# Performance work log

Hardware: AMD Instinct MI355X
Metric: run time of the kernel (lower is better)

## Reference

```python
import jax, jax.numpy as jnp
import numpy as np

H = 256; S = 64; AN = 16; D = 8; HH = 8; WW = 8; T = 32; N = 64; NV = 32
HG = 2 + 3 * H  # GRU hidden = sum(parser_sections) = 1 + 1 + 3*H


def _gru(x, w_ih, w_hh, b_ih, b_hh):
    """torch-style GRU over leading axis; x: [L, N, Hin] -> [L, N, HG]."""
    def step(h, xt):
        gi = xt @ w_ih.T + b_ih
        gh = h @ w_hh.T + b_hh
        ir, iz, inn = jnp.split(gi, 3, axis=-1)
        hr, hz, hn = jnp.split(gh, 3, axis=-1)
        r = jax.nn.sigmoid(ir + hr)
        z = jax.nn.sigmoid(iz + hz)
        n = jnp.tanh(inn + r * hn)
        h2 = (1 - z) * n + z * h
        return h2, h2
    h0 = jnp.zeros((x.shape[1], w_hh.shape[1]), x.dtype)
    _, ys = jax.lax.scan(step, h0, x)
    return ys


def _cos(e, m):  # e [N,H], m [N,S,H] -> [N,S]; matches F.cosine_similarity eps=1e-8
    num = jnp.einsum('nh,nsh->ns', e, m)
    den = jnp.linalg.norm(e, axis=-1)[:, None] * jnp.linalg.norm(m, axis=-1)
    return num / jnp.maximum(den, 1e-8)


def _l1norm(x):  # F.normalize(x, p=1, dim=-1)
    return x / jnp.maximum(jnp.abs(x).sum(-1, keepdims=True), 1e-12)


def setup_inputs():
    key = jax.random.key(0)
    ks = jax.random.split(key, 16)
    sc = lambda k, shape, fan: jax.random.normal(k, shape, jnp.float32) / np.float32(np.sqrt(fan))
    return dict(
        base=jax.random.normal(ks[0], (T, N, D, HH, WW), jnp.float32),
        interactable=(jax.random.uniform(ks[1], (T, N, AN - 5)) < 0.5).astype(jnp.float32),
        rnn_hxs=jnp.zeros((1, N, 1 + AN + 1 + H + S), jnp.float32),
        emb=sc(ks[2], (NV, H), 1.0),
        gru_w_ih=sc(ks[3], (3 * HG, H), H),
        gru_w_hh=sc(ks[4], (3 * HG, HG), HG),
        gru_b_ih=jnp.zeros((3 * HG,), jnp.float32),
        gru_b_hh=jnp.zeros((3 * HG,), jnp.float32),
        conv0_w=sc(ks[5], (H, D * H), D * H),
        conv0_b=jnp.zeros((H,), jnp.float32),
        convs_w=sc(ks[6], (2, H, H), H),
        convs_b=jnp.zeros((2, H), jnp.float32),
        lin_w=sc(ks[7], (H, H * HH * WW), H * HH * WW),
        lin_b=jnp.zeros((H,), jnp.float32),
        psi_w=sc(ks[8], (H, H * AN), H * AN),
        psi_b=jnp.zeros((H,), jnp.float32),
        actor_w=sc(ks[9], (AN, H), H),
        actor_b=jnp.zeros((AN,), jnp.float32),
        critic_w=sc(ks[10], (1, H), H),
        critic_b=jnp.zeros((1,), jnp.float32),
        subtasks=jax.random.randint(ks[11], (N, S), 0, NV),
        actions=jax.random.randint(ks[12], (T, N), 0, AN),
    )


def reference(base, interactable, rnn_hxs, emb, gru_w_ih, gru_w_hh, gru_b_ih, gru_b_hh,
              conv0_w, conv0_b, convs_w, convs_b, lin_w, lin_b, psi_w, psi_b,
              actor_w, actor_b, critic_w, critic_b, subtasks, actions):
    # --- parser: GRU over the subtask token sequence ---
    rnn_in = emb[subtasks].transpose(1, 0, 2)                                    # [S, N, H]
    X = _gru(rnn_in, gru_w_ih, gru_w_hh, gru_b_ih, gru_b_hh).transpose(1, 0, 2)  # [N, S, HG]
    c, p0 = X[..., 0], X[..., 1]                                                 # [N, S]
    M = X[..., 2:2 + H]
    Mm = X[..., 2 + H:2 + 2 * H]
    Mp = X[..., 2 + 2 * H:]
    hx = rnn_hxs[0]
    new_ep = jnp.all(rnn_hxs == 0, axis=-1)[0]                                   # [N]
    p_init = jnp.where(new_ep[:, None], p0, hx[:, 1 + AN + 1 + H:])

    def f_net(base_t, r):
        n = base_t.shape[0]
        # outer product [N,H,d,h,w] -> [N, H*d, h, w], then 1x1 convs
        x = (base_t[:, None] * r[:, :, None, None, None]).reshape(n, H * D, HH, WW)
        x = jax.nn.relu(jnp.einsum('nchw,oc->nohw', x, conv0_w) + conv0_b[None, :, None, None])
        for i in range(convs_w.shape[0]):
            x = jax.nn.relu(jnp.einsum('nchw,oc->nohw', x, convs_w[i]) + convs_b[i][None, :, None, None])
        return jax.nn.relu(x.reshape(n, -1) @ lin_w.T + lin_b)

    def step(p, xs):
        base_t, inter_t, a_t = xs
        ps = jax.nn.softmax(p, axis=-1)
        r = jnp.einsum('ns,nsh->nh', ps, M)                                      # memory read
        s = f_net(base_t, r)
        dprobs = jax.nn.softmax(s @ actor_w.T + actor_b, axis=-1)
        nonzero = jnp.pad(inter_t, ((0, 0), (5, 0)), constant_values=1.0)        # [N, AN]
        probs = dprobs * nonzero
        deficit = 1.0 - probs.sum(-1, keepdims=True)
        probs = probs + _l1norm(nonzero) * deficit
        probs = _l1norm(jnp.clip(probs, 0.0, 1.0))
        a_oh = jax.nn.one_hot(a_t, AN, dtype=s.dtype)
        e = (s[:, :, None] * a_oh[:, None, :]).reshape(s.shape[0], H * AN) @ psi_w.T + psi_b
        p_new = ps + c * _cos(e, Mp) - c * _cos(e, Mm)                           # memory write
        v = s @ critic_w.T + critic_b
        out = jnp.concatenate([a_t[:, None].astype(s.dtype), probs, v, s, p_new], axis=-1)
        return p_new, out

    _, hx_out = jax.lax.scan(step, p_init, (base, interactable, actions))        # [T, N, 338]
    return hx_out, hx_out[-1:]
```

## Files before the change

kernel.cpp:

```cpp
#include <hip/hip_runtime.h>
#include <math.h>

constexpr int cH  = 256;
constexpr int cS  = 64;
constexpr int cAN = 16;
constexpr int cD  = 8;
constexpr int cT  = 32;
constexpr int cN  = 64;
constexpr int cHG = 770;
constexpr int cG3 = 2310;
constexpr int cOW = 338;
constexpr int XLD = 800;
constexpr int GLD = 832;
constexpr int MLD = 2496;
constexpr int PROW = 2560;

__global__ __launch_bounds__(256) void k_gitab(const float* __restrict__ emb,
                                               const float* __restrict__ w_ih,
                                               const float* __restrict__ b_ih,
                                               float* __restrict__ gitp) {
  int v = blockIdx.y;
  int j = blockIdx.x * 256 + threadIdx.x;
  __shared__ float es[cH];
  es[threadIdx.x] = emb[v * cH + threadIdx.x];
  __syncthreads();
  if (j < cG3) {
    float acc = b_ih[j];
    const float* wr = w_ih + (size_t)j * cH;
    #pragma unroll 8
    for (int h = 0; h < cH; ++h) acc += wr[h] * es[h];
    int g = j / cHG, kk = j - g * cHG;
    gitp[(size_t)v * MLD + g * GLD + kk] = acc;
  }
}

__global__ __launch_bounds__(256) void k_wpad(const float* __restrict__ whh,
                                              float* __restrict__ wpadG) {
  int idx = blockIdx.x * 256 + threadIdx.x;
  if (idx < PROW * XLD) {
    int row = idx / XLD, col = idx - row * XLD;
    int g = row / GLD, k = row - g * GLD;
    wpadG[idx] = (g < 3 && k < cHG && col < cHG)
                     ? whh[(size_t)(g * cHG + k) * cHG + col] : 0.f;
  }
}

__global__ __launch_bounds__(256) void k_psiperm(const float* __restrict__ psi_w,
                                                 float* __restrict__ psip) {
  int idx = blockIdx.x * 256 + threadIdx.x;
  int a = idx >> 16, h = (idx >> 8) & 255, o = idx & 255;
  psip[idx] = psi_w[((size_t)o * cH + h) * cAN + a];
}

__global__ __launch_bounds__(256) void k_gru_gemm(const float* __restrict__ wpadG,
                                                  const float* __restrict__ X,
                                                  float* __restrict__ part, int s) {
  int tid = threadIdx.x;
  int tile = blockIdx.x % 40;
  int ks   = blockIdx.x / 40;
  int g = tile / 13, kt = tile - g * 13;
  int cbase = (ks <= 2) ? ks * 13 : 38;
  int ccnt  = (ks < 2) ? 13 : 12;
  int kbase = cbase * 16;
  int csz = ccnt * 16;

  __shared__ float Bst[208][68];
  __shared__ float As[2][16][68];

  const float* bsrc = wpadG + ((size_t)(g * GLD + kt * 64)) * XLD + kbase;
  for (int i = tid; i < 64 * 208; i += 256) {
    int jl = i / 208, k2l = i - jl * 208;
    if (k2l < csz) Bst[k2l][jl] = bsrc[(size_t)jl * XLD + k2l];
  }

  int tm = tid & 15, tj = tid >> 4;
  int lrow = tid >> 2, lcol = (tid & 3) * 4;
  __syncthreads();

  float acc[4][4] = {};
  const float* Xp = X + ((size_t)lrow * cS + (s - 1)) * XLD + kbase;
  float4 av = *(const float4*)(Xp + lcol);
  for (int c = 0; c < ccnt; ++c) {
    int buf = c & 1;
    As[buf][lcol + 0][lrow] = av.x;
    As[buf][lcol + 1][lrow] = av.y;
    As[buf][lcol + 2][lrow] = av.z;
    As[buf][lcol + 3][lrow] = av.w;
    __syncthreads();
    if (c + 1 < ccnt) av = *(const float4*)(Xp + (c + 1) * 16 + lcol);
    #pragma unroll
    for (int kk = 0; kk < 16; ++kk) {
      float4 a4 = *(const float4*)&As[buf][kk][tm * 4];
      float4 b4 = *(const float4*)&Bst[c * 16 + kk][tj * 4];
      acc[0][0] += a4.x * b4.x; acc[0][1] += a4.x * b4.y; acc[0][2] += a4.x * b4.z; acc[0][3] += a4.x * b4.w;
      acc[1][0] += a4.y * b4.x; acc[1][1] += a4.y * b4.y; acc[1][2] += a4.y * b4.z; acc[1][3] += a4.y * b4.w;
      acc[2][0] += a4.z * b4.x; acc[2][1] += a4.z * b4.y; acc[2][2] += a4.z * b4.z; acc[2][3] += a4.z * b4.w;
      acc[3][0] += a4.w * b4.x; acc[3][1] += a4.w * b4.y; acc[3][2] += a4.w * b4.z; acc[3][3] += a4.w * b4.w;
    }
    __syncthreads();
  }
  float* pw = part + (size_t)ks * (64 * PROW) + (size_t)(g * GLD + kt * 64);
  #pragma unroll
  for (int i = 0; i < 4; ++i) {
    *(float4*)(pw + (size_t)(tm * 4 + i) * PROW + tj * 4) =
        make_float4(acc[i][0], acc[i][1], acc[i][2], acc[i][3]);
  }
}

__global__ __launch_bounds__(256) void k_gru_gate(const float* __restrict__ part,
                                                  const float* __restrict__ bhh,
                                                  const float* __restrict__ gitp,
                                                  const int* __restrict__ subtasks,
                                                  float* __restrict__ X, int s) {
  int kq = blockIdx.x, m = blockIdx.y, tid = threadIdx.x;
  if (tid >= 200) return;
  int k = kq * 200 + tid;
  float* xrow = X + ((size_t)m * cS + s) * XLD;
  if (k >= cHG) { if (k < XLD) xrow[k] = 0.f; return; }
  float accr = 0.f, accz = 0.f, accn = 0.f;
  if (s > 0) {
    const float* pm = part + (size_t)m * PROW;
    #pragma unroll
    for (int q = 0; q < 4; ++q) {
      const float* pq = pm + (size_t)q * (64 * PROW);
      accr += pq[k];
      accz += pq[GLD + k];
      accn += pq[2 * GLD + k];
    }
  }
  int v = subtasks[m * cS + s];
  const float* git = gitp + (size_t)v * MLD;
  float rg = 1.f / (1.f + expf(-(git[k]           + accr + bhh[k])));
  float zg = 1.f / (1.f + expf(-(git[GLD + k]     + accz + bhh[cHG + k])));
  float ng = tanhf(git[2 * GLD + k] + rg * (accn + bhh[2 * cHG + k]));
  float hp = (s > 0) ? X[((size_t)m * cS + (s - 1)) * XLD + k] : 0.f;
  xrow[k] = (1.f - zg) * ng + zg * hp;
}

__global__ __launch_bounds__(256) void k_pinit(const float* __restrict__ hxs,
                                               const float* __restrict__ X,
                                               float* __restrict__ psb,
                                               float* __restrict__ r,
                                               float* __restrict__ nMp,
                                               float* __restrict__ nMm) {
  int n = blockIdx.x, tid = threadIdx.x;
  __shared__ int anynz;
  __shared__ float pss[cS];
  __shared__ float mx, sm;
  if (tid == 0) anynz = 0;
  __syncthreads();
  int nz = (hxs[n * cOW + tid] != 0.f) ? 1 : 0;
  if (tid + 256 < cOW) nz |= (hxs[n * cOW + tid + 256] != 0.f) ? 1 : 0;
  if (nz) anynz = 1;
  __syncthreads();
  bool newep = (anynz == 0);
  if (tid < cS) {
    const float* xr = X + ((size_t)n * cS + tid) * XLD;
    float p0 = xr[1];
    float pv = newep ? p0 : hxs[n * cOW + 1 + cAN + 1 + cH + tid];
    pss[tid] = pv;
    float sp = 0.f, smn = 0.f;
    for (int h = 0; h < cH; ++h) {
      float vp = xr[2 + 2 * cH + h]; sp += vp * vp;
      float vm = xr[2 + cH + h];     smn += vm * vm;
    }
    nMp[n * cS + tid] = sqrtf(sp);
    nMm[n * cS + tid] = sqrtf(smn);
  }
  __syncthreads();
  if (tid == 0) { float m = pss[0]; for (int i = 1; i < cS; ++i) m = fmaxf(m, pss[i]); mx = m; }
  __syncthreads();
  if (tid < cS) pss[tid] = expf(pss[tid] - mx);
  __syncthreads();
  if (tid == 0) { float s = 0.f; for (int i = 0; i < cS; ++i) s += pss[i]; sm = s; }
  __syncthreads();
  if (tid < cS) { pss[tid] /= sm; psb[n * cS + tid] = pss[tid]; }
  __syncthreads();
  float acc = 0.f;
  for (int s2 = 0; s2 < cS; ++s2)
    acc += pss[s2] * X[((size_t)n * cS + s2) * XLD + 2 + tid];
  r[n * cH + tid] = acc;
}

__global__ __launch_bounds__(256) void k_front(const float* __restrict__ r,
                                               const float* __restrict__ base,
                                               const float* __restrict__ cw,
                                               const float* __restrict__ cb,
                                               float* __restrict__ x1T, int t) {
  int o = blockIdx.x, tid = threadIdx.x;
  __shared__ float rsQ[64][65][4];
  __shared__ float w0s[64][9];

  #pragma unroll
  for (int it = 0; it < 16; ++it) {
    int flat4 = it * 256 + tid;
    int n = flat4 >> 6, hq = flat4 & 63;
    float4 v = *(const float4*)(r + n * cH + hq * 4);
    *(float4*)&rsQ[hq][n][0] = v;
  }
  __syncthreads();

  {
    int dg = tid >> 6, n = tid & 63;
    int d0 = dg * 2;
    const float* cwo = cw + (size_t)o * (cD * cH);
    float acc0 = 0.f, acc1 = 0.f;
    #pragma unroll 4
    for (int hq = 0; hq < 64; ++hq) {
      float4 rv = *(const float4*)&rsQ[hq][n][0];
      #pragma unroll
      for (int j = 0; j < 4; ++j) {
        float2 w = *(const float2*)(cwo + (hq * 4 + j) * 8 + d0);
        float rvj = ((const float*)&rv)[j];
        acc0 += w.x * rvj;
        acc1 += w.y * rvj;
      }
    }
    w0s[n][d0]     = acc0;
    w0s[n][d0 + 1] = acc1;
  }
  __syncthreads();

  {
    int q = tid >> 6, n = tid & 63;
    float w0[8];
    #pragma unroll
    for (int d = 0; d < 8; ++d) w0[d] = w0s[n][d];
    float bias = cb[o];
    const float4* b4 = (const float4*)(base + ((size_t)(t * cN + n) * cD) * 64);
    float* dst = x1T + (size_t)o * 4096 + n * 64 + q * 16;
    #pragma unroll
    for (int k = 0; k < 4; ++k) {
      float4 acc = make_float4(bias, bias, bias, bias);
      #pragma unroll
      for (int d = 0; d < 8; ++d) {
        float4 bv = b4[d * 16 + q * 4 + k];
        acc.x += w0[d] * bv.x; acc.y += w0[d] * bv.y;
        acc.z += w0[d] * bv.z; acc.w += w0[d] * bv.w;
      }
      acc.x = fmaxf(acc.x, 0.f); acc.y = fmaxf(acc.y, 0.f);
      acc.z = fmaxf(acc.z, 0.f); acc.w = fmaxf(acc.w, 0.f);
      *(float4*)(dst + k * 4) = acc;
    }
  }
}

__global__ __launch_bounds__(256) void k_gemmT(const float* __restrict__ AT,
                                               const float* __restrict__ W,
                                               const float* __restrict__ bias,
                                               float* __restrict__ C, int mode) {
  int nb = blockIdx.x, mb = blockIdx.y, tid = threadIdx.x;
  int tm = tid & 15, tj = tid >> 4;
  __shared__ float As[16][68];
  __shared__ float Bs[16][68];
  float acc[4][4] = {{0.f}};
  int lrow = tid >> 2, lcol = (tid & 3) * 4;
  int kr = tid >> 4, mc4 = (tid & 15) * 4;
  for (int kc = 0; kc < cH; kc += 16) {
    float4 av = *(const float4*)(AT + (size_t)(kc + kr) * 4096 + mb * 64 + mc4);
    float4 wv = *(const float4*)(W + (size_t)(nb * 64 + lrow) * cH + kc + lcol);
    *(float4*)&As[kr][mc4] = av;
    Bs[lcol][lrow] = wv.x; Bs[lcol + 1][lrow] = wv.y; Bs[lcol + 2][lrow] = wv.z; Bs[lcol + 3][lrow] = wv.w;
    __syncthreads();
    #pragma unroll
    for (int kk = 0; kk < 16; ++kk) {
      float4 a4 = *(const float4*)&As[kk][tm * 4];
      float4 b4 = *(const float4*)&Bs[kk][tj * 4];
      acc[0][0] += a4.x * b4.x; acc[0][1] += a4.x * b4.y; acc[0][2] += a4.x * b4.z; acc[0][3] += a4.x * b4.w;
      acc[1][0] += a4.y * b4.x; acc[1][1] += a4.y * b4.y; acc[1][2] += a4.y * b4.z; acc[1][3] += a4.y * b4.w;
      acc[2][0] += a4.z * b4.x; acc[2][1] += a4.z * b4.y; acc[2][2] += a4.z * b4.z; acc[2][3] += a4.z * b4.w;
      acc[3][0] += a4.w * b4.x; acc[3][1] += a4.w * b4.y; acc[3][2] += a4.w * b4.z; acc[3][3] += a4.w * b4.w;
    }
    __syncthreads();
  }
  if (mode == 0) {
    #pragma unroll
    for (int j = 0; j < 4; ++j) {
      int o = nb * 64 + tj * 4 + j;
      float bv = bias[o];
      float4 o4;
      o4.x = fmaxf(acc[0][j] + bv, 0.f);
      o4.y = fmaxf(acc[1][j] + bv, 0.f);
      o4.z = fmaxf(acc[2][j] + bv, 0.f);
      o4.w = fmaxf(acc[3][j] + bv, 0.f);
      *(float4*)(C + (size_t)o * 4096 + mb * 64 + tm * 4) = o4;
    }
  } else {
    #pragma unroll
    for (int j = 0; j < 4; ++j) {
      int o = nb * 64 + tj * 4 + j;
      float bv = bias[o];
      float4 o4;
      o4.x = fmaxf(acc[0][j] + bv, 0.f);
      o4.y = fmaxf(acc[1][j] + bv, 0.f);
      o4.z = fmaxf(acc[2][j] + bv, 0.f);
      o4.w = fmaxf(acc[3][j] + bv, 0.f);
      *(float4*)(C + (size_t)mb * (64 * cH) + (size_t)o * 64 + tm * 4) = o4;
    }
  }
}

__global__ __launch_bounds__(256) void k_lin(const float* __restrict__ A,
                                             const float* __restrict__ W,
                                             float* __restrict__ part) {
  int nb = blockIdx.x, kcb = blockIdx.y, tid = threadIdx.x;
  int tm = tid & 15, tj = tid >> 4;
  __shared__ float As[16][68];
  __shared__ float Bs[16][68];
  float acc[4][4] = {{0.f}};
  int lrow = tid >> 2, lcol = (tid & 3) * 4;
  for (int kc = 0; kc < 256; kc += 16) {
    float4 av = *(const float4*)(A + (size_t)lrow * 16384 + kcb * 256 + kc + lcol);
    float4 wv = *(const float4*)(W + (size_t)(nb * 64 + lrow) * 16384 + kcb * 256 + kc + lcol);
    As[lcol][lrow] = av.x; As[lcol + 1][lrow] = av.y; As[lcol + 2][lrow] = av.z; As[lcol + 3][lrow] = av.w;
    Bs[lcol][lrow] = wv.x; Bs[lcol + 1][lrow] = wv.y; Bs[lcol + 2][lrow] = wv.z; Bs[lcol + 3][lrow] = wv.w;
    __syncthreads();
    #pragma unroll
    for (int kk = 0; kk < 16; ++kk) {
      float4 a4 = *(const float4*)&As[kk][tm * 4];
      float4 b4 = *(const float4*)&Bs[kk][tj * 4];
      acc[0][0] += a4.x * b4.x; acc[0][1] += a4.x * b4.y; acc[0][2] += a4.x * b4.z; acc[0][3] += a4.x * b4.w;
      acc[1][0] += a4.y * b4.x; acc[1][1] += a4.y * b4.y; acc[1][2] += a4.y * b4.z; acc[1][3] += a4.y * b4.w;
      acc[2][0] += a4.z * b4.x; acc[2][1] += a4.z * b4.y; acc[2][2] += a4.z * b4.z; acc[2][3] += a4.z * b4.w;
      acc[3][0] += a4.w * b4.x; acc[3][1] += a4.w * b4.y; acc[3][2] += a4.w * b4.z; acc[3][3] += a4.w * b4.w;
    }
    __syncthreads();
  }
  #pragma unroll
  for (int i = 0; i < 4; ++i) {
    int n = tm * 4 + i;
    float4 o4 = make_float4(acc[i][0], acc[i][1], acc[i][2], acc[i][3]);
    *(float4*)(part + ((size_t)kcb * cN + n) * cH + nb * 64 + tj * 4) = o4;
  }
}

__global__ __launch_bounds__(256) void k_tail(const float* __restrict__ part,
                                              const float* __restrict__ lin_b,
                                              const float* __restrict__ actor_w,
                                              const float* __restrict__ actor_b,
                                              const float* __restrict__ critic_w,
                                              const float* __restrict__ critic_b,
                                              const float* __restrict__ psip,
                                              const float* __restrict__ psi_b,
                                              const float* __restrict__ inter,
                                              const int* __restrict__ actions,
                                              const float* __restrict__ X,
                                              const float* __restrict__ nMp,
                                              const float* __restrict__ nMm,
                                              float* __restrict__ psb,
                                              float* __restrict__ r,
                                              float* __restrict__ out, int t) {
  int n = blockIdx.x, tid = threadIdx.x;
  __shared__ float ss[cH];
  __shared__ float es[cH];
  __shared__ float lg[cAN], dp[cAN], nzv[cAN], prb[cAN];
  __shared__ float red[256];
  __shared__ float ared[16][17];
  __shared__ float cred[2][4][64];
  __shared__ float enorm_s;
  __shared__ float pns[cS];
  __shared__ float mx2, sm2;
  float* orow = out + ((size_t)t * cN + n) * cOW;
  float acc = lin_b[tid];
  for (int kc = 0; kc < 64; ++kc) acc += part[((size_t)kc * cN + n) * cH + tid];
  float sv = fmaxf(acc, 0.f);
  ss[tid] = sv;
  orow[1 + cAN + 1 + tid] = sv;
  __syncthreads();
  {
    int a = tid & 15, hg = tid >> 4;
    float pa = 0.f;
    const float* wr = actor_w + a * cH + hg * 16;
    const float* sh = &ss[hg * 16];
    #pragma unroll
    for (int hh2 = 0; hh2 < 16; ++hh2) pa += wr[hh2] * sh[hh2];
    ared[a][hg] = pa;
  }
  __syncthreads();
  if (tid < cAN) {
    float a = actor_b[tid];
    #pragma unroll
    for (int i = 0; i < 16; ++i) a += ared[tid][i];
    lg[tid] = a;
  }
  __syncthreads();
  if (tid < cAN) {
    float m = lg[0];
    for (int i = 1; i < cAN; ++i) m = fmaxf(m, lg[i]);
    dp[tid] = expf(lg[tid] - m);
  }
  __syncthreads();
  if (tid < cAN) {
    float s = 0.f;
    for (int i = 0; i < cAN; ++i) s += dp[i];
    float dprob = dp[tid] / s;
    float nv = (tid < 5) ? 1.f : inter[((size_t)t * cN + n) * (cAN - 5) + (tid - 5)];
    nzv[tid] = nv;
    prb[tid] = dprob * nv;
  }
  __syncthreads();
  if (tid < cAN) {
    float sp = 0.f, sn = 0.f;
    for (int i = 0; i < cAN; ++i) { sp += prb[i]; sn += nzv[i]; }
    float deficit = 1.f - sp;
    float v2 = prb[tid] + (nzv[tid] / fmaxf(sn, 1e-12f)) * deficit;
    prb[tid] = fminf(fmaxf(v2, 0.f), 1.f);
  }
  __syncthreads();
  if (tid < cAN) {
    float s = 0.f;
    for (int i = 0; i < cAN; ++i) s += prb[i];
    orow[1 + tid] = prb[tid] / fmaxf(s, 1e-12f);
  }
  int at = actions[t * cN + n];
  {
    float a = psi_b[tid];
    for (int h = 0; h < cH; ++h) a += psip[((size_t)at * cH + h) * cH + tid] * ss[h];
    es[tid] = a;
    red[tid] = a * a;
  }
  __syncthreads();
  for (int st = 128; st > 0; st >>= 1) {
    if (tid < st) red[tid] += red[tid + st];
    __syncthreads();
  }
  if (tid == 0) enorm_s = sqrtf(red[0]);
  __syncthreads();
  float enorm = enorm_s;
  red[tid] = critic_w[tid] * ss[tid];
  __syncthreads();
  for (int st = 128; st > 0; st >>= 1) {
    if (tid < st) red[tid] += red[tid + st];
    __syncthreads();
  }
  if (tid == 0) {
    orow[1 + cAN] = red[0] + critic_b[0];
    orow[0] = (float)at;
  }
  {
    int s2 = tid & 63, hg = tid >> 6;
    const float* xr = X + ((size_t)n * cS + s2) * XLD;
    const float* xp = xr + 2 + 2 * cH + hg * 64;
    const float* xm = xr + 2 + cH + hg * 64;
    const float* ep = &es[hg * 64];
    float dpp = 0.f, dmm = 0.f;
    #pragma unroll 8
    for (int h2 = 0; h2 < 64; ++h2) {
      float ev = ep[h2];
      dpp += ev * xp[h2];
      dmm += ev * xm[h2];
    }
    cred[0][hg][s2] = dpp;
    cred[1][hg][s2] = dmm;
  }
  __syncthreads();
  if (tid < cS) {
    float dpp = cred[0][0][tid] + cred[0][1][tid] + cred[0][2][tid] + cred[0][3][tid];
    float dmm = cred[1][0][tid] + cred[1][1][tid] + cred[1][2][tid] + cred[1][3][tid];
    const float* xr = X + ((size_t)n * cS + tid) * XLD;
    float cP = dpp / fmaxf(enorm * nMp[n * cS + tid], 1e-8f);
    float cM = dmm / fmaxf(enorm * nMm[n * cS + tid], 1e-8f);
    float cc = xr[0];
    float pn = psb[n * cS + tid] + cc * cP - cc * cM;
    pns[tid] = pn;
    orow[1 + cAN + 1 + cH + tid] = pn;
  }
  __threadfence_block();
  __syncthreads();
  if (t == cT - 1) {
    float* orow2 = out + (size_t)cT * cN * cOW + (size_t)n * cOW;
    orow2[tid] = orow[tid];
    if (tid + 256 < cOW) orow2[tid + 256] = orow[tid + 256];
  }
  if (tid == 0) { float m2 = pns[0]; for (int i = 1; i < cS; ++i) m2 = fmaxf(m2, pns[i]); mx2 = m2; }
  __syncthreads();
  if (tid < cS) pns[tid] = expf(pns[tid] - mx2);
  __syncthreads();
  if (tid == 0) { float s2 = 0.f; for (int i = 0; i < cS; ++i) s2 += pns[i]; sm2 = s2; }
  __syncthreads();
  if (tid < cS) { pns[tid] /= sm2; psb[n * cS + tid] = pns[tid]; }
  __syncthreads();
  float acc2 = 0.f;
  for (int s2 = 0; s2 < cS; ++s2)
    acc2 += pns[s2] * X[((size_t)n * cS + s2) * XLD + 2 + tid];
  r[n * cH + tid] = acc2;
}

extern "C" void kernel_launch(void* const* d_in, const int* in_sizes, int n_in,
                              void* d_out, int out_size, void* d_ws, size_t ws_size,
                              hipStream_t stream) {
  const float* base     = (const float*)d_in[0];
  const float* inter    = (const float*)d_in[1];
  const float* hxs      = (const float*)d_in[2];
  const float* emb      = (const float*)d_in[3];
  const float* w_ih     = (const float*)d_in[4];
  const float* w_hh     = (const float*)d_in[5];
  const float* b_ih     = (const float*)d_in[6];
  const float* b_hh     = (const float*)d_in[7];
  const float* conv0_w  = (const float*)d_in[8];
  const float* conv0_b  = (const float*)d_in[9];
  const float* convs_w  = (const float*)d_in[10];
  const float* convs_b  = (const float*)d_in[11];
  const float* lin_w    = (const float*)d_in[12];
  const float* lin_b    = (const float*)d_in[13];
  const float* psi_w    = (const float*)d_in[14];
  const float* psi_b    = (const float*)d_in[15];
  const float* actor_w  = (const float*)d_in[16];
  const float* actor_b  = (const float*)d_in[17];
  const float* critic_w = (const float*)d_in[18];
  const float* critic_b = (const float*)d_in[19];
  const int*   subtasks = (const int*)d_in[20];
  const int*   actions  = (const int*)d_in[21];
  float* out = (float*)d_out;
  float* ws  = (float*)d_ws;

  float* gitp  = ws + 0;
  float* psb   = ws + 0;
  float* r     = ws + 4096;
  float* nMp   = ws + 20480;
  float* nMm   = ws + 24576;
  float* X     = ws + 79872;
  float* wpadG = ws + 3356672;
  float* psip  = ws + 3356672;
  float* x1T   = ws + 4405248;
  float* part  = x1T;
  float* partG = ws + 5404672;
  float* x2T   = ws + 5453824;
  float* x3t   = ws + 6502400;

  k_gitab<<<dim3(10, 32), 256, 0, stream>>>(emb, w_ih, b_ih, gitp);
  k_wpad<<<8000, 256, 0, stream>>>(w_hh, wpadG);
  k_gru_gate<<<dim3(4, 64), 256, 0, stream>>>(partG, b_hh, gitp, subtasks, X, 0);
  for (int s = 1; s < cS; ++s) {
    k_gru_gemm<<<160, 256, 0, stream>>>(wpadG, X, partG, s);
    k_gru_gate<<<dim3(4, 64), 256, 0, stream>>>(partG, b_hh, gitp, subtasks, X, s);
  }
  k_psiperm<<<4096, 256, 0, stream>>>(psi_w, psip);
  k_pinit<<<64, 256, 0, stream>>>(hxs, X, psb, r, nMp, nMm);
  for (int t = 0; t < cT; ++t) {
    k_front<<<256, 256, 0, stream>>>(r, base, conv0_w, conv0_b, x1T, t);
    k_gemmT<<<dim3(4, 64), 256, 0, stream>>>(x1T, convs_w, convs_b, x2T, 0);
    k_gemmT<<<dim3(4, 64), 256, 0, stream>>>(x2T, convs_w + 65536, convs_b + 256, x3t, 1);
    k_lin<<<dim3(4, 64), 256, 0, stream>>>(x3t, lin_w, part);
    k_tail<<<64, 256, 0, stream>>>(part, lin_b, actor_w, actor_b, critic_w, critic_b,
                                   psip, psi_b, inter, actions, X, nMp, nMm,
                                   psb, r, out, t);
  }
}
```

Measured before the change: 4.611 ms.

## Fuse per-timestep kernels into one persistent kernel with grid barriers

Replaces the 160 per-timestep launches (front, two conv GEMMs, lin, tail) with one persistent 256-block kernel. Stages are separated by a two-level atomic grid barrier, and shared memory is held in a union across stages. This removes kernel launch and drain overhead across the 32-step recurrence. In exchange it relies on all 256 blocks being co-resident and adds barrier spin latency, and the tail stage leaves 192 blocks idle.

After: 12.71 ms. 176% more time.

```diff
diff --git a/kernel.cpp b/kernel.cpp
--- a/kernel.cpp
+++ b/kernel.cpp
@@ -35,8 +35,10 @@
 }
 
 __global__ __launch_bounds__(256) void k_wpad(const float* __restrict__ whh,
-                                              float* __restrict__ wpadG) {
+                                              float* __restrict__ wpadG,
+                                              unsigned* __restrict__ bar) {
   int idx = blockIdx.x * 256 + threadIdx.x;
+  if (idx < 16) bar[idx] = 0u;
   if (idx < PROW * XLD) {
     int row = idx / XLD, col = idx - row * XLD;
     int g = row / GLD, k = row - g * GLD;
@@ -182,308 +184,325 @@
   r[n * cH + tid] = acc;
 }
 
-__global__ __launch_bounds__(256) void k_front(const float* __restrict__ r,
-                                               const float* __restrict__ base,
-                                               const float* __restrict__ cw,
-                                               const float* __restrict__ cb,
-                                               float* __restrict__ x1T, int t) {
-  int o = blockIdx.x, tid = threadIdx.x;
-  __shared__ float rsQ[64][65][4];
-  __shared__ float w0s[64][9];
-
-  #pragma unroll
-  for (int it = 0; it < 16; ++it) {
-    int flat4 = it * 256 + tid;
-    int n = flat4 >> 6, hq = flat4 & 63;
-    float4 v = *(const float4*)(r + n * cH + hq * 4);
-    *(float4*)&rsQ[hq][n][0] = v;
-  }
-  __syncthreads();
-
-  {
-    int dg = tid >> 6, n = tid & 63;
-    int d0 = dg * 2;
-    const float* cwo = cw + (size_t)o * (cD * cH);
-    float acc0 = 0.f, acc1 = 0.f;
-    #pragma unroll 4
-    for (int hq = 0; hq < 64; ++hq) {
-      float4 rv = *(const float4*)&rsQ[hq][n][0];
+struct FrontS { float rsQ[64][65][4]; float w0s[64][9]; };
+struct GemmS  { float As[16][68]; float Bs[16][68]; };
+struct TailS  {
+  float ss[cH]; float es[cH];
+  float lg[cAN], dp[cAN], nzv[cAN], prb[cAN];
+  float red[256]; float ared[16][17]; float cred[2][4][64];
+  float enorm_s; float pns[cS]; float mx2, sm2;
+};
+union MegaS { FrontS f; GemmS g; TailS t; };
+
+__device__ __forceinline__ void gbar(unsigned* sub, unsigned* root, int b, int ph) {
+  __syncthreads();
+  if (threadIdx.x == 0) {
+    __threadfence();
+    unsigned v = __hip_atomic_fetch_add(&sub[b & 7], 1u, __ATOMIC_ACQ_REL,
+                                        __HIP_MEMORY_SCOPE_AGENT) + 1u;
+    if (v == (unsigned)(32 * (ph + 1)))
+      __hip_atomic_fetch_add(root, 1u, __ATOMIC_ACQ_REL, __HIP_MEMORY_SCOPE_AGENT);
+    while (__hip_atomic_load(root, __ATOMIC_ACQUIRE, __HIP_MEMORY_SCOPE_AGENT) <
+           (unsigned)(8 * (ph + 1))) {
+      __builtin_amdgcn_s_sleep(2);
+    }
+  }
+  __syncthreads();
+}
+
+__global__ __launch_bounds__(256) void k_mega(
+    const float* __restrict__ base, const float* __restrict__ inter,
+    const float* __restrict__ cw0, const float* __restrict__ cb0,
+    const float* __restrict__ convs_w, const float* __restrict__ convs_b,
+    const float* __restrict__ lin_w, const float* __restrict__ lin_b,
+    const float* __restrict__ actor_w, const float* __restrict__ actor_b,
+    const float* __restrict__ critic_w, const float* __restrict__ critic_b,
+    const float* __restrict__ psip, const float* __restrict__ psi_b,
+    const int* __restrict__ actions, const float* __restrict__ X,
+    const float* __restrict__ nMp, const float* __restrict__ nMm,
+    float* __restrict__ psb, float* __restrict__ r,
+    float* __restrict__ x1T, float* __restrict__ x2T, float* __restrict__ x3t,
+    float* __restrict__ out, unsigned* __restrict__ bar) {
+  __shared__ MegaS sm;
+  int b = blockIdx.x, tid = threadIdx.x;
+  unsigned* sub = bar;
+  unsigned* root = bar + 8;
+  float* part = x1T;
+  int ph = 0;
+
+  for (int t = 0; t < cT; ++t) {
+    {
+      int o = b;
       #pragma unroll
-      for (int j = 0; j < 4; ++j) {
-        float2 w = *(const float2*)(cwo + (hq * 4 + j) * 8 + d0);
-        float rvj = ((const float*)&rv)[j];
-        acc0 += w.x * rvj;
-        acc1 += w.y * rvj;
-      }
-    }
-    w0s[n][d0]     = acc0;
-    w0s[n][d0 + 1] = acc1;
-  }
-  __syncthreads();
-
-  {
-    int q = tid >> 6, n = tid & 63;
-    float w0[8];
-    #pragma unroll
-    for (int d = 0; d < 8; ++d) w0[d] = w0s[n][d];
-    float bias = cb[o];
-    const float4* b4 = (const float4*)(base + ((size_t)(t * cN + n) * cD) * 64);
-    float* dst = x1T + (size_t)o * 4096 + n * 64 + q * 16;
-    #pragma unroll
-    for (int k = 0; k < 4; ++k) {
-      float4 acc = make_float4(bias, bias, bias, bias);
+      for (int it = 0; it < 16; ++it) {
+        int flat4 = it * 256 + tid;
+        int n = flat4 >> 6, hq = flat4 & 63;
+        float4 v = *(const float4*)(r + n * cH + hq * 4);
+        *(float4*)&sm.f.rsQ[hq][n][0] = v;
+      }
+      __syncthreads();
+      {
+        int dg = tid >> 6, n = tid & 63;
+        int d0 = dg * 2;
+        const float* cwo = cw0 + (size_t)o * (cD * cH);
+        float acc0 = 0.f, acc1 = 0.f;
+        #pragma unroll 4
+        for (int hq = 0; hq < 64; ++hq) {
+          float4 rv = *(const float4*)&sm.f.rsQ[hq][n][0];
+          #pragma unroll
+          for (int j = 0; j < 4; ++j) {
+            float2 w = *(const float2*)(cwo + (hq * 4 + j) * 8 + d0);
+            float rvj = ((const float*)&rv)[j];
+            acc0 += w.x * rvj;
+            acc1 += w.y * rvj;
+          }
+        }
+        sm.f.w0s[n][d0]     = acc0;
+        sm.f.w0s[n][d0 + 1] = acc1;
+      }
+      __syncthreads();
+      {
+        int q = tid >> 6, n = tid & 63;
+        float w0[8];
+        #pragma unroll
+        for (int d = 0; d < 8; ++d) w0[d] = sm.f.w0s[n][d];
+        float bias = cb0[o];
+        const float4* b4 = (const float4*)(base + ((size_t)(t * cN + n) * cD) * 64);
+        float* dst = x1T + (size_t)o * 4096 + n * 64 + q * 16;
+        #pragma unroll
+        for (int k = 0; k < 4; ++k) {
+          float4 acc = make_float4(bias, bias, bias, bias);
+          #pragma unroll
+          for (int d = 0; d < 8; ++d) {
+            float4 bv = b4[d * 16 + q * 4 + k];
+            acc.x += w0[d] * bv.x; acc.y += w0[d] * bv.y;
+            acc.z += w0[d] * bv.z; acc.w += w0[d] * bv.w;
+          }
+          acc.x = fmaxf(acc.x, 0.f); acc.y = fmaxf(acc.y, 0.f);
+          acc.z = fmaxf(acc.z, 0.f); acc.w = fmaxf(acc.w, 0.f);
+          *(float4*)(dst + k * 4) = acc;
+        }
+      }
+    }
+    gbar(sub, root, b, ph++);
+
+    for (int cv = 0; cv < 2; ++cv) {
+      const float* AT  = (cv == 0) ? x1T : x2T;
+      const float* W   = convs_w + cv * 65536;
+      const float* bia = convs_b + cv * 256;
+      int nb = b >> 6, mb = b & 63;
+      int tm = tid & 15, tj = tid >> 4;
+      float acc[4][4] = {{0.f}};
+      int lrow = tid >> 2, lcol = (tid & 3) * 4;
+      int kr = tid >> 4, mc4 = (tid & 15) * 4;
+      for (int kc = 0; kc < cH; kc += 16) {
+        float4 av = *(const float4*)(AT + (size_t)(kc + kr) * 4096 + mb * 64 + mc4);
+        float4 wv = *(const float4*)(W + (size_t)(nb * 64 + lrow) * cH + kc + lcol);
+        *(float4*)&sm.g.As[kr][mc4] = av;
+        sm.g.Bs[lcol][lrow] = wv.x; sm.g.Bs[lcol + 1][lrow] = wv.y;
+        sm.g.Bs[lcol + 2][lrow] = wv.z; sm.g.Bs[lcol + 3][lrow] = wv.w;
+        __syncthreads();
+        #pragma unroll
+        for (int kk = 0; kk < 16; ++kk) {
+          float4 a4 = *(const float4*)&sm.g.As[kk][tm * 4];
+          float4 b4 = *(const float4*)&sm.g.Bs[kk][tj * 4];
+          acc[0][0] += a4.x * b4.x; acc[0][1] += a4.x * b4.y; acc[0][2] += a4.x * b4.z; acc[0][3] += a4.x * b4.w;
+          acc[1][0] += a4.y * b4.x; acc[1][1] += a4.y * b4.y; acc[1][2] += a4.y * b4.z; acc[1][3] += a4.y * b4.w;
+          acc[2][0] += a4.z * b4.x; acc[2][1] += a4.z * b4.y; acc[2][2] += a4.z * b4.z; acc[2][3] += a4.z * b4.w;
+          acc[3][0] += a4.w * b4.x; acc[3][1] += a4.w * b4.y; acc[3][2] += a4.w * b4.z; acc[3][3] += a4.w * b4.w;
+        }
+        __syncthreads();
+      }
+      if (cv == 0) {
+        #pragma unroll
+        for (int j = 0; j < 4; ++j) {
+          int o = nb * 64 + tj * 4 + j;
+          float bv = bia[o];
+          float4 o4;
+          o4.x = fmaxf(acc[0][j] + bv, 0.f);
+          o4.y = fmaxf(acc[1][j] + bv, 0.f);
+          o4.z = fmaxf(acc[2][j] + bv, 0.f);
+          o4.w = fmaxf(acc[3][j] + bv, 0.f);
+          *(float4*)(x2T + (size_t)o * 4096 + mb * 64 + tm * 4) = o4;
+        }
+      } else {
+        #pragma unroll
+        for (int j = 0; j < 4; ++j) {
+          int o = nb * 64 + tj * 4 + j;
+          float bv = bia[o];
+          float4 o4;
+          o4.x = fmaxf(acc[0][j] + bv, 0.f);
+          o4.y = fmaxf(acc[1][j] + bv, 0.f);
+          o4.z = fmaxf(acc[2][j] + bv, 0.f);
+          o4.w = fmaxf(acc[3][j] + bv, 0.f);
+          *(float4*)(x3t + (size_t)mb * (64 * cH) + (size_t)o * 64 + tm * 4) = o4;
+        }
+      }
+      gbar(sub, root, b, ph++);
+    }
+
+    {
+      int nb = b >> 6, kcb = b & 63;
+      int tm = tid & 15, tj = tid >> 4;
+      float acc[4][4] = {{0.f}};
+      int lrow = tid >> 2, lcol = (tid & 3) * 4;
+      for (int kc = 0; kc < 256; kc += 16) {
+        float4 av = *(const float4*)(x3t + (size_t)lrow * 16384 + kcb * 256 + kc + lcol);
+        float4 wv = *(const float4*)(lin_w + (size_t)(nb * 64 + lrow) * 16384 + kcb * 256 + kc + lcol);
+        sm.g.As[lcol][lrow] = av.x; sm.g.As[lcol + 1][lrow] = av.y;
+        sm.g.As[lcol + 2][lrow] = av.z; sm.g.As[lcol + 3][lrow] = av.w;
+        sm.g.Bs[lcol][lrow] = wv.x; sm.g.Bs[lcol + 1][lrow] = wv.y;
+        sm.g.Bs[lcol + 2][lrow] = wv.z; sm.g.Bs[lcol + 3][lrow] = wv.w;
+        __syncthreads();
+        #pragma unroll
+        for (int kk = 0; kk < 16; ++kk) {
+          float4 a4 = *(const float4*)&sm.g.As[kk][tm * 4];
+          float4 b4 = *(const float4*)&sm.g.Bs[kk][tj * 4];
+          acc[0][0] += a4.x * b4.x; acc[0][1] += a4.x * b4.y; acc[0][2] += a4.x * b4.z; acc[0][3] += a4.x * b4.w;
+          acc[1][0] += a4.y * b4.x; acc[1][1] += a4.y * b4.y; acc[1][2] += a4.y * b4.z; acc[1][3] += a4.y * b4.w;
+          acc[2][0] += a4.z * b4.x; acc[2][1] += a4.z * b4.y; acc[2][2] += a4.z * b4.z; acc[2][3] += a4.z * b4.w;
+          acc[3][0] += a4.w * b4.x; acc[3][1] += a4.w * b4.y; acc[3][2] += a4.w * b4.z; acc[3][3] += a4.w * b4.w;
+        }
+        __syncthreads();
+      }
       #pragma unroll
-      for (int d = 0; d < 8; ++d) {
-        float4 bv = b4[d * 16 + q * 4 + k];
-        acc.x += w0[d] * bv.x; acc.y += w0[d] * bv.y;
-        acc.z += w0[d] * bv.z; acc.w += w0[d] * bv.w;
-      }
-      acc.x = fmaxf(acc.x, 0.f); acc.y = fmaxf(acc.y, 0.f);
-      acc.z = fmaxf(acc.z, 0.f); acc.w = fmaxf(acc.w, 0.f);
-      *(float4*)(dst + k * 4) = acc;
-    }
-  }
-}
-
-__global__ __launch_bounds__(256) void k_gemmT(const float* __restrict__ AT,
-                                               const float* __restrict__ W,
-                                               const float* __restrict__ bias,
-                                               float* __restrict__ C, int mode) {
-  int nb = blockIdx.x, mb = blockIdx.y, tid = threadIdx.x;
-  int tm = tid & 15, tj = tid >> 4;
-  __shared__ float As[16][68];
-  __shared__ float Bs[16][68];
-  float acc[4][4] = {{0.f}};
-  int lrow = tid >> 2, lcol = (tid & 3) * 4;
-  int kr = tid >> 4, mc4 = (tid & 15) * 4;
-  for (int kc = 0; kc < cH; kc += 16) {
-    float4 av = *(const float4*)(AT + (size_t)(kc + kr) * 4096 + mb * 64 + mc4);
-    float4 wv = *(const float4*)(W + (size_t)(nb * 64 + lrow) * cH + kc + lcol);
-    *(float4*)&As[kr][mc4] = av;
-    Bs[lcol][lrow] = wv.x; Bs[lcol + 1][lrow] = wv.y; Bs[lcol + 2][lrow] = wv.z; Bs[lcol + 3][lrow] = wv.w;
-    __syncthreads();
-    #pragma unroll
-    for (int kk = 0; kk < 16; ++kk) {
-      float4 a4 = *(const float4*)&As[kk][tm * 4];
-      float4 b4 = *(const float4*)&Bs[kk][tj * 4];
-      acc[0][0] += a4.x * b4.x; acc[0][1] += a4.x * b4.y; acc[0][2] += a4.x * b4.z; acc[0][3] += a4.x * b4.w;
-      acc[1][0] += a4.y * b4.x; acc[1][1] += a4.y * b4.y; acc[1][2] += a4.y * b4.z; acc[1][3] += a4.y * b4.w;
-      acc[2][0] += a4.z * b4.x; acc[2][1] += a4.z * b4.y; acc[2][2] += a4.z * b4.z; acc[2][3] += a4.z * b4.w;
-      acc[3][0] += a4.w * b4.x; acc[3][1] += a4.w * b4.y; acc[3][2] += a4.w * b4.z; acc[3][3] += a4.w * b4.w;
-    }
-    __syncthreads();
-  }
-  if (mode == 0) {
-    #pragma unroll
-    for (int j = 0; j < 4; ++j) {
-      int o = nb * 64 + tj * 4 + j;
-      float bv = bias[o];
-      float4 o4;
-      o4.x = fmaxf(acc[0][j] + bv, 0.f);
-      o4.y = fmaxf(acc[1][j] + bv, 0.f);
-      o4.z = fmaxf(acc[2][j] + bv, 0.f);
-      o4.w = fmaxf(acc[3][j] + bv, 0.f);
-      *(float4*)(C + (size_t)o * 4096 + mb * 64 + tm * 4) = o4;
-    }
-  } else {
-    #pragma unroll
-    for (int j = 0; j < 4; ++j) {
-      int o = nb * 64 + tj * 4 + j;
-      float bv = bias[o];
-      float4 o4;
-      o4.x = fmaxf(acc[0][j] + bv, 0.f);
-      o4.y = fmaxf(acc[1][j] + bv, 0.f);
-      o4.z = fmaxf(acc[2][j] + bv, 0.f);
-      o4.w = fmaxf(acc[3][j] + bv, 0.f);
-      *(float4*)(C + (size_t)mb * (64 * cH) + (size_t)o * 64 + tm * 4) = o4;
-    }
-  }
-}
-
-__global__ __launch_bounds__(256) void k_lin(const float* __restrict__ A,
-                                             const float* __restrict__ W,
-                                             float* __restrict__ part) {
-  int nb = blockIdx.x, kcb = blockIdx.y, tid = threadIdx.x;
-  int tm = tid & 15, tj = tid >> 4;
-  __shared__ float As[16][68];
-  __shared__ float Bs[16][68];
-  float acc[4][4] = {{0.f}};
-  int lrow = tid >> 2, lcol = (tid & 3) * 4;
-  for (int kc = 0; kc < 256; kc += 16) {
-    float4 av = *(const float4*)(A + (size_t)lrow * 16384 + kcb * 256 + kc + lcol);
-    float4 wv = *(const float4*)(W + (size_t)(nb * 64 + lrow) * 16384 + kcb * 256 + kc + lcol);
-    As[lcol][lrow] = av.x; As[lcol + 1][lrow] = av.y; As[lcol + 2][lrow] = av.z; As[lcol + 3][lrow] = av.w;
-    Bs[lcol][lrow] = wv.x; Bs[lcol + 1][lrow] = wv.y; Bs[lcol + 2][lrow] = wv.z; Bs[lcol + 3][lrow] = wv.w;
-    __syncthreads();
-    #pragma unroll
-    for (int kk = 0; kk < 16; ++kk) {
-      float4 a4 = *(const float4*)&As[kk][tm * 4];
-      float4 b4 = *(const float4*)&Bs[kk][tj * 4];
-      acc[0][0] += a4.x * b4.x; acc[0][1] += a4.x * b4.y; acc[0][2] += a4.x * b4.z; acc[0][3] += a4.x * b4.w;
-      acc[1][0] += a4.y * b4.x; acc[1][1] += a4.y * b4.y; acc[1][2] += a4.y * b4.z; acc[1][3] += a4.y * b4.w;
-      acc[2][0] += a4.z * b4.x; acc[2][1] += a4.z * b4.y; acc[2][2] += a4.z * b4.z; acc[2][3] += a4.z * b4.w;
-      acc[3][0] += a4.w * b4.x; acc[3][1] += a4.w * b4.y; acc[3][2] += a4.w * b4.z; acc[3][3] += a4.w * b4.w;
-    }
-    __syncthreads();
-  }
-  #pragma unroll
-  for (int i = 0; i < 4; ++i) {
-    int n = tm * 4 + i;
-    float4 o4 = make_float4(acc[i][0], acc[i][1], acc[i][2], acc[i][3]);
-    *(float4*)(part + ((size_t)kcb * cN + n) * cH + nb * 64 + tj * 4) = o4;
-  }
-}
-
-__global__ __launch_bounds__(256) void k_tail(const float* __restrict__ part,
-                                              const float* __restrict__ lin_b,
-                                              const float* __restrict__ actor_w,
-                                              const float* __restrict__ actor_b,
-                                              const float* __restrict__ critic_w,
-                                              const float* __restrict__ critic_b,
-                                              const float* __restrict__ psip,
-                                              const float* __restrict__ psi_b,
-                                              const float* __restrict__ inter,
-                                              const int* __restrict__ actions,
-                                              const float* __restrict__ X,
-                                              const float* __restrict__ nMp,
-                                              const float* __restrict__ nMm,
-                                              float* __restrict__ psb,
-                                              float* __restrict__ r,
-                                              float* __restrict__ out, int t) {
-  int n = blockIdx.x, tid = threadIdx.x;
-  __shared__ float ss[cH];
-  __shared__ float es[cH];
-  __shared__ float lg[cAN], dp[cAN], nzv[cAN], prb[cAN];
-  __shared__ float red[256];
-  __shared__ float ared[16][17];
-  __shared__ float cred[2][4][64];
-  __shared__ float enorm_s;
-  __shared__ float pns[cS];
-  __shared__ float mx2, sm2;
-  float* orow = out + ((size_t)t * cN + n) * cOW;
-  float acc = lin_b[tid];
-  for (int kc = 0; kc < 64; ++kc) acc += part[((size_t)kc * cN + n) * cH + tid];
-  float sv = fmaxf(acc, 0.f);
-  ss[tid] = sv;
-  orow[1 + cAN + 1 + tid] = sv;
-  __syncthreads();
-  {
-    int a = tid & 15, hg = tid >> 4;
-    float pa = 0.f;
-    const float* wr = actor_w + a * cH + hg * 16;
-    const float* sh = &ss[hg * 16];
-    #pragma unroll
-    for (int hh2 = 0; hh2 < 16; ++hh2) pa += wr[hh2] * sh[hh2];
-    ared[a][hg] = pa;
-  }
-  __syncthreads();
-  if (tid < cAN) {
-    float a = actor_b[tid];
-    #pragma unroll
-    for (int i = 0; i < 16; ++i) a += ared[tid][i];
-    lg[tid] = a;
-  }
-  __syncthreads();
-  if (tid < cAN) {
-    float m = lg[0];
-    for (int i = 1; i < cAN; ++i) m = fmaxf(m, lg[i]);
-    dp[tid] = expf(lg[tid] - m);
-  }
-  __syncthreads();
-  if (tid < cAN) {
-    float s = 0.f;
-    for (int i = 0; i < cAN; ++i) s += dp[i];
-    float dprob = dp[tid] / s;
-    float nv = (tid < 5) ? 1.f : inter[((size_t)t * cN + n) * (cAN - 5) + (tid - 5)];
-    nzv[tid] = nv;
-    prb[tid] = dprob * nv;
-  }
-  __syncthreads();
-  if (tid < cAN) {
-    float sp = 0.f, sn = 0.f;
-    for (int i = 0; i < cAN; ++i) { sp += prb[i]; sn += nzv[i]; }
-    float deficit = 1.f - sp;
-    float v2 = prb[tid] + (nzv[tid] / fmaxf(sn, 1e-12f)) * deficit;
-    prb[tid] = fminf(fmaxf(v2, 0.f), 1.f);
-  }
-  __syncthreads();
-  if (tid < cAN) {
-    float s = 0.f;
-    for (int i = 0; i < cAN; ++i) s += prb[i];
-    orow[1 + tid] = prb[tid] / fmaxf(s, 1e-12f);
-  }
-  int at = actions[t * cN + n];
-  {
-    float a = psi_b[tid];
-    for (int h = 0; h < cH; ++h) a += psip[((size_t)at * cH + h) * cH + tid] * ss[h];
-    es[tid] = a;
-    red[tid] = a * a;
-  }
-  __syncthreads();
-  for (int st = 128; st > 0; st >>= 1) {
-    if (tid < st) red[tid] += red[tid + st];
-    __syncthreads();
-  }
-  if (tid == 0) enorm_s = sqrtf(red[0]);
-  __syncthreads();
-  float enorm = enorm_s;
-  red[tid] = critic_w[tid] * ss[tid];
-  __syncthreads();
-  for (int st = 128; st > 0; st >>= 1) {
-    if (tid < st) red[tid] += red[tid + st];
-    __syncthreads();
-  }
-  if (tid == 0) {
-    orow[1 + cAN] = red[0] + critic_b[0];
-    orow[0] = (float)at;
-  }
-  {
-    int s2 = tid & 63, hg = tid >> 6;
-    const float* xr = X + ((size_t)n * cS + s2) * XLD;
-    const float* xp = xr + 2 + 2 * cH + hg * 64;
-    const float* xm = xr + 2 + cH + hg * 64;
-    const float* ep = &es[hg * 64];
-    float dpp = 0.f, dmm = 0.f;
-    #pragma unroll 8
-    for (int h2 = 0; h2 < 64; ++h2) {
-      float ev = ep[h2];
-      dpp += ev * xp[h2];
-      dmm += ev * xm[h2];
-    }
-    cred[0][hg][s2] = dpp;
-    cred[1][hg][s2] = dmm;
-  }
-  __syncthreads();
-  if (tid < cS) {
-    float dpp = cred[0][0][tid] + cred[0][1][tid] + cred[0][2][tid] + cred[0][3][tid];
-    float dmm = cred[1][0][tid] + cred[1][1][tid] + cred[1][2][tid] + cred[1][3][tid];
-    const float* xr = X + ((size_t)n * cS + tid) * XLD;
-    float cP = dpp / fmaxf(enorm * nMp[n * cS + tid], 1e-8f);
-    float cM = dmm / fmaxf(enorm * nMm[n * cS + tid], 1e-8f);
-    float cc = xr[0];
-    float pn = psb[n * cS + tid] + cc * cP - cc * cM;
-    pns[tid] = pn;
-    orow[1 + cAN + 1 + cH + tid] = pn;
-  }
-  __threadfence_block();
-  __syncthreads();
-  if (t == cT - 1) {
-    float* orow2 = out + (size_t)cT * cN * cOW + (size_t)n * cOW;
-    orow2[tid] = orow[tid];
-    if (tid + 256 < cOW) orow2[tid + 256] = orow[tid + 256];
-  }
-  if (tid == 0) { float m2 = pns[0]; for (int i = 1; i < cS; ++i) m2 = fmaxf(m2, pns[i]); mx2 = m2; }
-  __syncthreads();
-  if (tid < cS) pns[tid] = expf(pns[tid] - mx2);
-  __syncthreads();
-  if (tid == 0) { float s2 = 0.f; for (int i = 0; i < cS; ++i) s2 += pns[i]; sm2 = s2; }
-  __syncthreads();
-  if (tid < cS) { pns[tid] /= sm2; psb[n * cS + tid] = pns[tid]; }
-  __syncthreads();
-  float acc2 = 0.f;
-  for (int s2 = 0; s2 < cS; ++s2)
-    acc2 += pns[s2] * X[((size_t)n * cS + s2) * XLD + 2 + tid];
-  r[n * cH + tid] = acc2;
+      for (int i = 0; i < 4; ++i) {
+        int n = tm * 4 + i;
+        float4 o4 = make_float4(acc[i][0], acc[i][1], acc[i][2], acc[i][3]);
+        *(float4*)(part + ((size_t)kcb * cN + n) * cH + nb * 64 + tj * 4) = o4;
+      }
+    }
+    gbar(sub, root, b, ph++);
+
+    if (b < cN) {
+      int n = b;
+      float* orow = out + ((size_t)t * cN + n) * cOW;
+      float acc = lin_b[tid];
+      for (int kc = 0; kc < 64; ++kc) acc += part[((size_t)kc * cN + n) * cH + tid];
+      float sv = fmaxf(acc, 0.f);
+      sm.t.ss[tid] = sv;
+      orow[1 + cAN + 1 + tid] = sv;
+      __syncthreads();
+      {
+        int a = tid & 15, hg = tid >> 4;
+        float pa = 0.f;
+        const float* wr = actor_w + a * cH + hg * 16;
+        const float* sh = &sm.t.ss[hg * 16];
+        #pragma unroll
+        for (int hh2 = 0; hh2 < 16; ++hh2) pa += wr[hh2] * sh[hh2];
+        sm.t.ared[a][hg] = pa;
+      }
+      __syncthreads();
+      if (tid < cAN) {
+        float a = actor_b[tid];
+        #pragma unroll
+        for (int i = 0; i < 16; ++i) a += sm.t.ared[tid][i];
+        sm.t.lg[tid] = a;
+      }
+      __syncthreads();
+      if (tid < cAN) {
+        float m = sm.t.lg[0];
+        for (int i = 1; i < cAN; ++i) m = fmaxf(m, sm.t.lg[i]);
+        sm.t.dp[tid] = expf(sm.t.lg[tid] - m);
+      }
+      __syncthreads();
+      if (tid < cAN) {
+        float s = 0.f;
+        for (int i = 0; i < cAN; ++i) s += sm.t.dp[i];
+        float dprob = sm.t.dp[tid] / s;
+        float nv = (tid < 5) ? 1.f : inter[((size_t)t * cN + n) * (cAN - 5) + (tid - 5)];
+        sm.t.nzv[tid] = nv;
+        sm.t.prb[tid] = dprob * nv;
+      }
+      __syncthreads();
+      if (tid < cAN) {
+        float sp = 0.f, sn = 0.f;
+        for (int i = 0; i < cAN; ++i) { sp += sm.t.prb[i]; sn += sm.t.nzv[i]; }
+        float deficit = 1.f - sp;
+        float v2 = sm.t.prb[tid] + (sm.t.nzv[tid] / fmaxf(sn, 1e-12f)) * deficit;
+        sm.t.prb[tid] = fminf(fmaxf(v2, 0.f), 1.f);
+      }
+      __syncthreads();
+      if (tid < cAN) {
+        float s = 0.f;
+        for (int i = 0; i < cAN; ++i) s += sm.t.prb[i];
+        orow[1 + tid] = sm.t.prb[tid] / fmaxf(s, 1e-12f);
+      }
+      int at = actions[t * cN + n];
+      {
+        float a = psi_b[tid];
+        for (int h = 0; h < cH; ++h) a += psip[((size_t)at * cH + h) * cH + tid] * sm.t.ss[h];
+        sm.t.es[tid] = a;
+        sm.t.red[tid] = a * a;
+      }
+      __syncthreads();
+      for (int st = 128; st > 0; st >>= 1) {
+        if (tid < st) sm.t.red[tid] += sm.t.red[tid + st];
+        __syncthreads();
+      }
+      if (tid == 0) sm.t.enorm_s = sqrtf(sm.t.red[0]);
+      __syncthreads();
+      float enorm = sm.t.enorm_s;
+      sm.t.red[tid] = critic_w[tid] * sm.t.ss[tid];
+      __syncthreads();
+      for (int st = 128; st > 0; st >>= 1) {
+        if (tid < st) sm.t.red[tid] += sm.t.red[tid + st];
+        __syncthreads();
+      }
+      if (tid == 0) {
+        orow[1 + cAN] = sm.t.red[0] + critic_b[0];
+        orow[0] = (float)at;
+      }
+      {
+        int s2 = tid & 63, hg = tid >> 6;
+        const float* xr = X + ((size_t)n * cS + s2) * XLD;
+        const float* xp = xr + 2 + 2 * cH + hg * 64;
+        const float* xm = xr + 2 + cH + hg * 64;
+        const float* ep = &sm.t.es[hg * 64];
+        float dpp = 0.f, dmm = 0.f;
+        #pragma unroll 8
+        for (int h2 = 0; h2 < 64; ++h2) {
+          float ev = ep[h2];
+          dpp += ev * xp[h2];
+          dmm += ev * xm[h2];
+        }
+        sm.t.cred[0][hg][s2] = dpp;
+        sm.t.cred[1][hg][s2] = dmm;
+      }
+      __syncthreads();
+      if (tid < cS) {
+        float dpp = sm.t.cred[0][0][tid] + sm.t.cred[0][1][tid] + sm.t.cred[0][2][tid] + sm.t.cred[0][3][tid];
+        float dmm = sm.t.cred[1][0][tid] + sm.t.cred[1][1][tid] + sm.t.cred[1][2][tid] + sm.t.cred[1][3][tid];
+        const float* xr = X + ((size_t)n * cS + tid) * XLD;
+        float cP = dpp / fmaxf(enorm * nMp[n * cS + tid], 1e-8f);
+        float cM = dmm / fmaxf(enorm * nMm[n * cS + tid], 1e-8f);
+        float cc = xr[0];
+        float pn = psb[n * cS + tid] + cc * cP - cc * cM;
+        sm.t.pns[tid] = pn;
+        orow[1 + cAN + 1 + cH + tid] = pn;
+      }
+      __threadfence_block();
+      __syncthreads();
+      if (t == cT - 1) {
+        float* orow2 = out + (size_t)cT * cN * cOW + (size_t)n * cOW;
+        orow2[tid] = orow[tid];
+        if (tid + 256 < cOW) orow2[tid + 256] = orow[tid + 256];
+      }
+      if (tid == 0) { float m2 = sm.t.pns[0]; for (int i = 1; i < cS; ++i) m2 = fmaxf(m2, sm.t.pns[i]); sm.t.mx2 = m2; }
+      __syncthreads();
+      if (tid < cS) sm.t.pns[tid] = expf(sm.t.pns[tid] - sm.t.mx2);
+      __syncthreads();
+      if (tid == 0) { float s2 = 0.f; for (int i = 0; i < cS; ++i) s2 += sm.t.pns[i]; sm.t.sm2 = s2; }
+      __syncthreads();
+      if (tid < cS) { sm.t.pns[tid] /= sm.t.sm2; psb[n * cS + tid] = sm.t.pns[tid]; }
+      __syncthreads();
+      float acc2 = 0.f;
+      for (int s2 = 0; s2 < cS; ++s2)
+        acc2 += sm.t.pns[s2] * X[((size_t)n * cS + s2) * XLD + 2 + tid];
+      r[n * cH + tid] = acc2;
+    }
+    gbar(sub, root, b, ph++);
+  }
 }
 
 extern "C" void kernel_launch(void* const* d_in, const int* in_sizes, int n_in,
@@ -514,22 +533,22 @@
   float* out = (float*)d_out;
   float* ws  = (float*)d_ws;
 
-  float* gitp  = ws + 0;
-  float* psb   = ws + 0;
-  float* r     = ws + 4096;
-  float* nMp   = ws + 20480;
-  float* nMm   = ws + 24576;
-  float* X     = ws + 79872;
-  float* wpadG = ws + 3356672;
-  float* psip  = ws + 3356672;
-  float* x1T   = ws + 4405248;
-  float* part  = x1T;
-  float* partG = ws + 5404672;
-  float* x2T   = ws + 5453824;
-  float* x3t   = ws + 6502400;
+  float* gitp   = ws + 0;
+  float* psb    = ws + 0;
+  float* r      = ws + 4096;
+  float* nMp    = ws + 20480;
+  float* nMm    = ws + 24576;
+  float* X      = ws + 79872;
+  float* wpadG  = ws + 3356672;
+  float* psip   = ws + 3356672;
+  float* x1T    = ws + 4405248;
+  float* partG  = ws + 5404672;
+  float* x2T    = ws + 5453824;
+  float* x3t    = ws + 6502400;
+  unsigned* bar = (unsigned*)(ws + 7550976);
 
   k_gitab<<<dim3(10, 32), 256, 0, stream>>>(emb, w_ih, b_ih, gitp);
-  k_wpad<<<8000, 256, 0, stream>>>(w_hh, wpadG);
+  k_wpad<<<8000, 256, 0, stream>>>(w_hh, wpadG, bar);
   k_gru_gate<<<dim3(4, 64), 256, 0, stream>>>(partG, b_hh, gitp, subtasks, X, 0);
   for (int s = 1; s < cS; ++s) {
     k_gru_gemm<<<160, 256, 0, stream>>>(wpadG, X, partG, s);
@@ -537,13 +556,8 @@
   }
   k_psiperm<<<4096, 256, 0, stream>>>(psi_w, psip);
   k_pinit<<<64, 256, 0, stream>>>(hxs, X, psb, r, nMp, nMm);
-  for (int t = 0; t < cT; ++t) {
-    k_front<<<256, 256, 0, stream>>>(r, base, conv0_w, conv0_b, x1T, t);
-    k_gemmT<<<dim3(4, 64), 256, 0, stream>>>(x1T, convs_w, convs_b, x2T, 0);
-    k_gemmT<<<dim3(4, 64), 256, 0, stream>>>(x2T, convs_w + 65536, convs_b + 256, x3t, 1);
-    k_lin<<<dim3(4, 64), 256, 0, stream>>>(x3t, lin_w, part);
-    k_tail<<<64, 256, 0, stream>>>(part, lin_b, actor_w, actor_b, critic_w, critic_b,
-                                   psip, psi_b, inter, actions, X, nMp, nMm,
-                                   psb, r, out, t);
-  }
-}
+  k_mega<<<256, 256, 0, stream>>>(base, inter, conv0_w, conv0_b, convs_w, convs_b,
+                                  lin_w, lin_b, actor_w, actor_b, critic_w, critic_b,
+                                  psip, psi_b, actions, X, nMp, nMm,
+                                  psb, r, x1T, x2T, x3t, out, bar);
+}
```
